# Kernel optimization log

Hardware: AMD Instinct MI355X
Metric: run time of the kernel (lower is better)

## Reference

```python
import jax, jax.numpy as jnp
import numpy as np

DIM = 768
HID = 1536
EPS = 1e-12
SCALE = float(np.sqrt(DIM))


def _layernorm(x, gamma, beta):
    mu = jnp.mean(x, axis=-1, keepdims=True)
    var = jnp.mean(jnp.square(x - mu), axis=-1, keepdims=True)
    return (x - mu) * jax.lax.rsqrt(var + EPS) * gamma + beta


def setup_inputs() -> dict:
    key = jax.random.key(0)
    ks = jax.random.split(key, 16)
    s = 1.0 / np.sqrt(DIM)
    sh = 1.0 / np.sqrt(HID)
    x = jax.random.normal(ks[0], (8, 2048, DIM), dtype=jnp.float32)
    return {
        "x": x,
        "Wq": jax.random.uniform(ks[1], (DIM, DIM), jnp.float32, -s, s),
        "bq": jax.random.uniform(ks[2], (DIM,), jnp.float32, -s, s),
        "Wk": jax.random.uniform(ks[3], (DIM, DIM), jnp.float32, -s, s),
        "bk": jax.random.uniform(ks[4], (DIM,), jnp.float32, -s, s),
        "Wv": jax.random.uniform(ks[5], (DIM, DIM), jnp.float32, -s, s),
        "bv": jax.random.uniform(ks[6], (DIM,), jnp.float32, -s, s),
        "Wp": jax.random.uniform(ks[7], (DIM, DIM), jnp.float32, -s, s),
        "bp": jax.random.uniform(ks[8], (DIM,), jnp.float32, -s, s),
        "g1": jnp.ones((DIM,), jnp.float32),
        "be1": jnp.zeros((DIM,), jnp.float32),
        "W1": jax.random.uniform(ks[9], (HID, DIM), jnp.float32, -s, s),
        "b1": jax.random.uniform(ks[10], (HID,), jnp.float32, -s, s),
        "W2": jax.random.uniform(ks[11], (DIM, HID), jnp.float32, -sh, sh),
        "b2": jax.random.uniform(ks[12], (DIM,), jnp.float32, -sh, sh),
        "g2": jnp.ones((DIM,), jnp.float32),
        "be2": jnp.zeros((DIM,), jnp.float32),
    }


def reference(x, Wq, bq, Wk, bk, Wv, bv, Wp, bp, g1, be1, W1, b1, W2, b2, g2, be2):
    # NOTE: original code does NOT split into heads; single full-dim bmm attention.
    Q = jnp.einsum("bsd,ed->bse", x, Wq) + bq  # [B,S,D]
    K = jnp.einsum("bsd,ed->bse", x, Wk) + bk
    V = jnp.einsum("bsd,ed->bse", x, Wv) + bv
    alpha = jnp.einsum("bqd,bkd->bqk", Q, K) / SCALE  # [B,S,S]
    alpha = jax.nn.softmax(alpha, axis=-1)
    attn = jnp.einsum("bqk,bkd->bqd", alpha, V)
    attn = jnp.einsum("bsd,ed->bse", attn, Wp) + bp  # linear_proj
    h = _layernorm(x + attn, g1, be1)
    mlp = jax.nn.gelu(jnp.einsum("bsd,hd->bsh", h, W1) + b1, approximate=False)
    mlp = jnp.einsum("bsh,dh->bsd", mlp, W2) + b2
    return _layernorm(h + mlp, g2, be2)
```

## Files before the change

### kernel.cpp

```cpp
#include <hip/hip_runtime.h>
#include <math.h>

#define D_MODEL 768
#define D_HID   1536
#define N_BATCH 8
#define SEQLEN  2048
#define NROWS   (N_BATCH*SEQLEN)

typedef unsigned short u16;
typedef __attribute__((ext_vector_type(8))) short bfrag;
typedef __attribute__((ext_vector_type(4))) float facc;

__device__ __forceinline__ u16 f2bf(float f) {
  unsigned u = __float_as_uint(f);
  u += 0x7fffu + ((u >> 16) & 1u);
  return (u16)(u >> 16);
}
__device__ __forceinline__ float bf2f(u16 u) {
  return __uint_as_float((unsigned)u << 16);
}

__device__ __forceinline__ void async16(const void* g, void* l) {
  __builtin_amdgcn_global_load_lds((const __attribute__((address_space(1))) void*)g,
                                   (__attribute__((address_space(3))) void*)l,
                                   16, 0, 0);
}

__global__ __launch_bounds__(256) void cvt_all(
    const float* __restrict__ x,  const float* __restrict__ Wq,
    const float* __restrict__ Wk, const float* __restrict__ Wv,
    const float* __restrict__ Wp, const float* __restrict__ W1,
    const float* __restrict__ W2, const float* __restrict__ bq,
    const float* __restrict__ bk, const float* __restrict__ bv,
    u16* __restrict__ XB, u16* __restrict__ WQKV, u16* __restrict__ WPB,
    u16* __restrict__ W1B, u16* __restrict__ W2B, float* __restrict__ BQKV) {
  long i = (long)blockIdx.x * 256 + threadIdx.x;
  const float* src; u16* dst; long off;
  if      (i < 3145728) { src = x;  dst = XB;             off = i; }
  else if (i < 3293184) { src = Wq; dst = WQKV;           off = i - 3145728; }
  else if (i < 3440640) { src = Wk; dst = WQKV + 589824;  off = i - 3293184; }
  else if (i < 3588096) { src = Wv; dst = WQKV + 1179648; off = i - 3440640; }
  else if (i < 3735552) { src = Wp; dst = WPB;            off = i - 3588096; }
  else if (i < 4030464) { src = W1; dst = W1B;            off = i - 3735552; }
  else if (i < 4325376) { src = W2; dst = W2B;            off = i - 4030464; }
  else if (i < 4325952) {
    long j = i - 4325376;
    const float* s = (j < 192) ? bq : (j < 384) ? bk : bv;
    long o = (j < 192) ? j : (j < 384) ? j - 192 : j - 384;
    ((float4*)BQKV)[j] = ((const float4*)s)[o];
    return;
  } else return;
  float4 v = ((const float4*)src)[off];
  ushort4 o4;
  o4.x = f2bf(v.x); o4.y = f2bf(v.y); o4.z = f2bf(v.z); o4.w = f2bf(v.w);
  *reinterpret_cast<ushort4*>(dst + off * 4) = o4;
}

__global__ __launch_bounds__(256) void transpose_bf16(const u16* __restrict__ in,
                                                      u16* __restrict__ out) {
  __shared__ u16 t[64][68];
  const int z  = blockIdx.z;
  const int bs = blockIdx.x * 64;
  const int bd = blockIdx.y * 64;
  const u16* I = in  + (long)z * SEQLEN * D_MODEL;
  u16*       O = out + (long)z * D_MODEL * SEQLEN;
  const int tt = threadIdx.x;
  const int r = tt >> 2, c4 = (tt & 3) << 4;
#pragma unroll
  for (int k = 0; k < 16; ++k)
    t[r][c4 + k] = I[(long)(bs + r) * D_MODEL + bd + c4 + k];
  __syncthreads();
#pragma unroll
  for (int k = 0; k < 16; ++k)
    O[(long)(bd + r) * SEQLEN + bs + c4 + k] = t[c4 + k][r];
}

enum { EPI_EXP = 1, EPI_DIV = 2, EPI_GELU = 4, EPI_QKV = 5, EPI_RES = 6 };

template<int EPI>
__global__ __launch_bounds__(512, 4)
void gemm_bt(const u16* __restrict__ Aall, const u16* __restrict__ Ball,
             void* __restrict__ Cout,
             int M, int N, int K,
             long sA, long sB, long sC,
             const float* __restrict__ bias,
             const u16* __restrict__ resid,
             float* __restrict__ lsum,
             float scale)
{
  __shared__ __align__(16) char smem[65536];
  u16* As = (u16*)smem;
  u16* Bs = (u16*)(smem + 16384);

  const int z = blockIdx.z;
  const u16* A = Aall + (long)z * sA;
  const u16* B = Ball + (long)z * sB;
  const int bm = blockIdx.x, bn = blockIdx.y;
  const int tid = (int)threadIdx.x;
  const int lane = tid & 63, wv = tid >> 6;
  const int wr = wv >> 2, wc = wv & 3;

  facc acc[4][4] = {};

  const int srow = tid >> 3;
  const int scol = (((tid & 7) ^ (srow & 7)) << 3);
  const u16* Abase = A + (long)(bm * 128) * K;
  const u16* Bbase = B + (long)(bn * 256) * K;

  const int fr = lane & 15;
  const int g0 = lane >> 4;

  for (int k0 = 0; k0 < K; k0 += 64) {
    __syncthreads();
#pragma unroll
    for (int p = 0; p < 2; ++p)
      async16(Abase + (long)(p * 64 + srow) * K + k0 + scol, As + (p * 512 + wv * 64) * 8);
#pragma unroll
    for (int p = 0; p < 4; ++p)
      async16(Bbase + (long)(p * 64 + srow) * K + k0 + scol, Bs + (p * 512 + wv * 64) * 8);
    __syncthreads();
#pragma unroll
    for (int h = 0; h < 2; ++h) {
      bfrag af[4], bfv[4];
      const int gh = g0 + h * 4;
#pragma unroll
      for (int i = 0; i < 4; ++i) {
        const int r = wr * 64 + i * 16 + fr;
        af[i] = *(const bfrag*)(As + r * 64 + ((gh ^ (r & 7)) << 3));
      }
#pragma unroll
      for (int j = 0; j < 4; ++j) {
        const int r = wc * 64 + j * 16 + fr;
        bfv[j] = *(const bfrag*)(Bs + r * 64 + ((gh ^ (r & 7)) << 3));
      }
#pragma unroll
      for (int i = 0; i < 4; ++i)
#pragma unroll
        for (int j = 0; j < 4; ++j)
          acc[i][j] = __builtin_amdgcn_mfma_f32_16x16x32_bf16(af[i], bfv[j], acc[i][j], 0, 0, 0);
    }
  }

  __syncthreads();
  const int rb = bm * 128 + wr * 64;
  const int cb = bn * 256 + wc * 64;
  const int quad = lane >> 4;

  if constexpr (EPI == EPI_RES) {
    float* ep32 = (float*)(smem + wv * 8192);
    u16* Cg = (u16*)Cout;
#pragma unroll
    for (int h = 0; h < 2; ++h) {
#pragma unroll
      for (int i2 = 0; i2 < 2; ++i2) {
        const int i = h * 2 + i2;
#pragma unroll
        for (int r = 0; r < 4; ++r) {
          const int lrow = i2 * 16 + quad * 4 + r;
#pragma unroll
          for (int j = 0; j < 4; ++j)
            ep32[lrow * 64 + j * 16 + fr] = acc[i][j][r];
        }
      }
#pragma unroll
      for (int it = 0; it < 8; ++it) {
        const int lr = it * 4 + (lane >> 4);
        const int ch = (lane & 15) << 2;
        float4 d = *(const float4*)(ep32 + lr * 64 + ch);
        const int row = rb + h * 32 + lr;
        const int gcol = cb + ch;
        const long gi = (long)row * N + gcol;
        ushort4 rv = *(const ushort4*)(resid + gi);
        float4 bb = *(const float4*)(bias + gcol);
        ushort4 o;
        o.x = f2bf(d.x + bb.x + bf2f(rv.x));
        o.y = f2bf(d.y + bb.y + bf2f(rv.y));
        o.z = f2bf(d.z + bb.z + bf2f(rv.z));
        o.w = f2bf(d.w + bb.w + bf2f(rv.w));
        *reinterpret_cast<ushort4*>(Cg + gi) = o;
      }
    }
  } else {
    u16* ep16 = (u16*)(smem + wv * 8192);
    u16* Cg;
    int cbo, rowstride;
    if constexpr (EPI == EPI_QKV) {
      const int c64 = bn * 4 + wc;
      const int which = c64 / 12;
      Cg = (u16*)Cout + (long)which * NROWS * D_MODEL;
      cbo = (c64 - which * 12) * 64;
      rowstride = D_MODEL;
    } else {
      Cg = (u16*)Cout + (long)z * sC;
      cbo = cb;
      rowstride = N;
    }
    float bj[4];
    if constexpr (EPI == EPI_GELU || EPI == EPI_QKV) {
#pragma unroll
      for (int j = 0; j < 4; ++j) bj[j] = bias[cb + j * 16 + fr];
    }
#pragma unroll
    for (int i = 0; i < 4; ++i) {
#pragma unroll
      for (int r = 0; r < 4; ++r) {
        const int lrow = i * 16 + quad * 4 + r;
        const int row = rb + lrow;
        float rs = 0.f;
        float inv = 0.f;
        if constexpr (EPI == EPI_DIV) inv = 1.f / lsum[(long)z * M + row];
#pragma unroll
        for (int j = 0; j < 4; ++j) {
          float v = acc[i][j][r];
          float outv;
          if constexpr (EPI == EPI_EXP) {
            outv = __expf(v * scale);
            rs += outv;
          } else if constexpr (EPI == EPI_DIV) {
            outv = v * inv;
          } else if constexpr (EPI == EPI_QKV) {
            outv = v + bj[j];
          } else {
            float t = v + bj[j];
            outv = 0.5f * t * (1.f + erff(t * 0.70710678f));
          }
          ep16[lrow * 64 + j * 16 + fr] = f2bf(outv);
        }
        if constexpr (EPI == EPI_EXP) {
          rs += __shfl_xor(rs, 1);
          rs += __shfl_xor(rs, 2);
          rs += __shfl_xor(rs, 4);
          rs += __shfl_xor(rs, 8);
          if (fr == 0) atomicAdd(&lsum[(long)z * M + row], rs);
        }
      }
    }
#pragma unroll
    for (int it = 0; it < 8; ++it) {
      const int lr = it * 8 + (lane >> 3);
      const int ch = (lane & 7) << 3;
      int4 d = *(const int4*)(ep16 + lr * 64 + ch);
      *reinterpret_cast<int4*>(Cg + (long)(rb + lr) * rowstride + cbo + ch) = d;
    }
  }
}

__global__ __launch_bounds__(192) void layernorm_rows(const u16* __restrict__ in,
                                                      const float* __restrict__ gamma,
                                                      const float* __restrict__ beta,
                                                      float* __restrict__ outf,
                                                      u16* __restrict__ outb) {
  const int row = blockIdx.x;
  const int t = threadIdx.x;
  ushort4 uv = ((const ushort4*)(in + (long)row * D_MODEL))[t];
  float v0 = bf2f(uv.x), v1 = bf2f(uv.y), v2 = bf2f(uv.z), v3 = bf2f(uv.w);
  float s1 = v0 + v1 + v2 + v3;
  float s2 = v0 * v0 + v1 * v1 + v2 * v2 + v3 * v3;
#pragma unroll
  for (int o = 32; o; o >>= 1) { s1 += __shfl_xor(s1, o); s2 += __shfl_xor(s2, o); }
  __shared__ float r1[3], r2[3];
  const int wv = t >> 6, ln = t & 63;
  if (ln == 0) { r1[wv] = s1; r2[wv] = s2; }
  __syncthreads();
  s1 = r1[0] + r1[1] + r1[2];
  s2 = r2[0] + r2[1] + r2[2];
  const float mu = s1 * (1.f / 768.f);
  const float var = s2 * (1.f / 768.f) - mu * mu;
  const float rstd = rsqrtf(var + 1e-12f);
  float4 gv = ((const float4*)gamma)[t];
  float4 bv = ((const float4*)beta)[t];
  float o0 = (v0 - mu) * rstd * gv.x + bv.x;
  float o1 = (v1 - mu) * rstd * gv.y + bv.y;
  float o2 = (v2 - mu) * rstd * gv.z + bv.z;
  float o3 = (v3 - mu) * rstd * gv.w + bv.w;
  if (outf) {
    float4 ov = {o0, o1, o2, o3};
    ((float4*)(outf + (long)row * D_MODEL))[t] = ov;
  }
  if (outb) {
    ushort4 ob;
    ob.x = f2bf(o0); ob.y = f2bf(o1); ob.z = f2bf(o2); ob.w = f2bf(o3);
    ((ushort4*)(outb + (long)row * D_MODEL))[t] = ob;
  }
}

static const size_t OFF_WP   = 0;
static const size_t OFF_W1   = 1179648;
static const size_t OFF_W2   = 3538944;
static const size_t OFF_LSUM = 5898240;
static const size_t OFF_BQKV = 5963776;
static const size_t OFF_QB   = 6291456;
static const size_t OFF_KB   = 31457280;
static const size_t OFF_VB   = 56623104;
static const size_t OFF_VT   = 81788928;
static const size_t OFF_EB   = 106954752;
static const size_t OFF_XB   = 174063616;
static const size_t OFF_WQKV = 199229440;

extern "C" void kernel_launch(void* const* d_in, const int* in_sizes, int n_in,
                              void* d_out, int out_size, void* d_ws, size_t ws_size,
                              hipStream_t stream) {
  const float* x   = (const float*)d_in[0];
  const float* Wq  = (const float*)d_in[1];
  const float* bq  = (const float*)d_in[2];
  const float* Wk  = (const float*)d_in[3];
  const float* bk  = (const float*)d_in[4];
  const float* Wv  = (const float*)d_in[5];
  const float* bv  = (const float*)d_in[6];
  const float* Wp  = (const float*)d_in[7];
  const float* bp  = (const float*)d_in[8];
  const float* g1  = (const float*)d_in[9];
  const float* be1 = (const float*)d_in[10];
  const float* W1  = (const float*)d_in[11];
  const float* b1  = (const float*)d_in[12];
  const float* W2  = (const float*)d_in[13];
  const float* b2  = (const float*)d_in[14];
  const float* g2  = (const float*)d_in[15];
  const float* be2 = (const float*)d_in[16];

  char* ws = (char*)d_ws;
  u16*   WPB  = (u16*)(ws + OFF_WP);
  u16*   W1B  = (u16*)(ws + OFF_W1);
  u16*   W2B  = (u16*)(ws + OFF_W2);
  float* LSUM = (float*)(ws + OFF_LSUM);
  float* BQKV = (float*)(ws + OFF_BQKV);
  u16*   QB   = (u16*)(ws + OFF_QB);
  u16*   KB   = (u16*)(ws + OFF_KB);
  u16*   VB   = (u16*)(ws + OFF_VB);
  u16*   VT   = (u16*)(ws + OFF_VT);
  u16*   EB   = (u16*)(ws + OFF_EB);
  u16*   XB   = (u16*)(ws + OFF_XB);
  u16*   WQKV = (u16*)(ws + OFF_WQKV);
  u16*   CTX  = (u16*)(ws + OFF_VB);
  u16*   PB   = (u16*)(ws + OFF_QB);
  u16*   HB   = (u16*)(ws + OFF_EB);
  u16*   M1B  = (u16*)(ws + OFF_QB);
  u16*   M2B  = (u16*)(ws + OFF_VT);

  dim3 blk(256), blkg(512), blkl(192);

  cvt_all<<<dim3(16899), blk, 0, stream>>>(x, Wq, Wk, Wv, Wp, W1, W2, bq, bk, bv,
                                           XB, WQKV, WPB, W1B, W2B, BQKV);
  hipMemsetAsync(LSUM, 0, NROWS * sizeof(float), stream);

  gemm_bt<EPI_QKV><<<dim3(128, 9, 1), blkg, 0, stream>>>(XB, WQKV, QB,
      NROWS, 3 * D_MODEL, D_MODEL, 0, 0, 0, BQKV, nullptr, nullptr, 0.f);
  transpose_bf16<<<dim3(SEQLEN / 64, D_MODEL / 64, N_BATCH), blk, 0, stream>>>(VB, VT);

  const float sc = 1.0f / sqrtf((float)D_MODEL);
  gemm_bt<EPI_EXP><<<dim3(16, 8, 8), blkg, 0, stream>>>(QB, KB, EB,
      SEQLEN, SEQLEN, D_MODEL,
      (long)SEQLEN * D_MODEL, (long)SEQLEN * D_MODEL, (long)SEQLEN * SEQLEN,
      nullptr, nullptr, LSUM, sc);
  gemm_bt<EPI_DIV><<<dim3(16, 3, 8), blkg, 0, stream>>>(EB, VT, CTX,
      SEQLEN, D_MODEL, SEQLEN,
      (long)SEQLEN * SEQLEN, (long)D_MODEL * SEQLEN, (long)SEQLEN * D_MODEL,
      nullptr, nullptr, LSUM, 0.f);
  gemm_bt<EPI_RES><<<dim3(128, 3, 1), blkg, 0, stream>>>(CTX, WPB, PB,
      NROWS, D_MODEL, D_MODEL, 0, 0, 0, bp, XB, nullptr, 0.f);
  layernorm_rows<<<dim3(NROWS), blkl, 0, stream>>>(PB, g1, be1, nullptr, HB);
  gemm_bt<EPI_GELU><<<dim3(128, 6, 1), blkg, 0, stream>>>(HB, W1B, M1B,
      NROWS, D_HID, D_MODEL, 0, 0, 0, b1, nullptr, nullptr, 0.f);
  gemm_bt<EPI_RES><<<dim3(128, 3, 1), blkg, 0, stream>>>(M1B, W2B, M2B,
      NROWS, D_MODEL, D_HID, 0, 0, 0, b2, HB, nullptr, 0.f);
  layernorm_rows<<<dim3(NROWS), blkl, 0, stream>>>(M2B, g2, be2, (float*)d_out, nullptr);

  (void)in_sizes; (void)n_in; (void)out_size; (void)ws_size;
}
```

Before: 485.3 us.

## Fuse V transpose into QKV epilogue and use 128x128 tiles for N=768 GEMMs

The QKV GEMM epilogue now writes the V third directly in transposed [dim][seq] layout, which removes the separate transpose kernel and one round trip of V through global memory. A new 256-thread gemm_bt128 kernel with 128x128 tiles and 32KB LDS replaces the 128x256 kernel for the three GEMMs with N=768, doubling their grid size so the CUs are better filled. In exchange, the transposed V stores are narrow strided 8-byte writes, and the smaller tiles reuse each loaded operand less.

```diff
diff --git a/kernel.cpp b/kernel.cpp
--- a/kernel.cpp
+++ b/kernel.cpp
@@ -56,25 +56,6 @@
   *reinterpret_cast<ushort4*>(dst + off * 4) = o4;
 }
 
-__global__ __launch_bounds__(256) void transpose_bf16(const u16* __restrict__ in,
-                                                      u16* __restrict__ out) {
-  __shared__ u16 t[64][68];
-  const int z  = blockIdx.z;
-  const int bs = blockIdx.x * 64;
-  const int bd = blockIdx.y * 64;
-  const u16* I = in  + (long)z * SEQLEN * D_MODEL;
-  u16*       O = out + (long)z * D_MODEL * SEQLEN;
-  const int tt = threadIdx.x;
-  const int r = tt >> 2, c4 = (tt & 3) << 4;
-#pragma unroll
-  for (int k = 0; k < 16; ++k)
-    t[r][c4 + k] = I[(long)(bs + r) * D_MODEL + bd + c4 + k];
-  __syncthreads();
-#pragma unroll
-  for (int k = 0; k < 16; ++k)
-    O[(long)(bd + r) * SEQLEN + bs + c4 + k] = t[c4 + k][r];
-}
-
 enum { EPI_EXP = 1, EPI_DIV = 2, EPI_GELU = 4, EPI_QKV = 5, EPI_RES = 6 };
 
 template<int EPI>
@@ -144,6 +125,165 @@
   __syncthreads();
   const int rb = bm * 128 + wr * 64;
   const int cb = bn * 256 + wc * 64;
+  const int quad = lane >> 4;
+
+  if constexpr (EPI == EPI_QKV) {
+    const int c64 = bn * 4 + wc;
+    const int which = c64 / 12;
+    float bj[4];
+#pragma unroll
+    for (int j = 0; j < 4; ++j) bj[j] = bias[cb + j * 16 + fr];
+    if (which == 2) {
+      u16* VT_ = (u16*)resid;
+      const int zb = rb >> 11;
+      const int seqb = (rb & 2047) + quad * 4;
+      const int dimb = (c64 - 24) * 64;
+#pragma unroll
+      for (int i = 0; i < 4; ++i) {
+#pragma unroll
+        for (int j = 0; j < 4; ++j) {
+          const int dim = dimb + j * 16 + fr;
+          ushort4 o;
+          o.x = f2bf(acc[i][j][0] + bj[j]);
+          o.y = f2bf(acc[i][j][1] + bj[j]);
+          o.z = f2bf(acc[i][j][2] + bj[j]);
+          o.w = f2bf(acc[i][j][3] + bj[j]);
+          *reinterpret_cast<ushort4*>(VT_ + (long)zb * D_MODEL * SEQLEN +
+                                      (long)dim * SEQLEN + seqb + i * 16) = o;
+        }
+      }
+      return;
+    }
+    u16* ep16 = (u16*)(smem + wv * 8192);
+    u16* Cg = (u16*)Cout + (long)which * NROWS * D_MODEL;
+    const int cbo = (c64 - which * 12) * 64;
+#pragma unroll
+    for (int i = 0; i < 4; ++i)
+#pragma unroll
+      for (int r = 0; r < 4; ++r) {
+        const int lrow = i * 16 + quad * 4 + r;
+#pragma unroll
+        for (int j = 0; j < 4; ++j)
+          ep16[lrow * 64 + j * 16 + fr] = f2bf(acc[i][j][r] + bj[j]);
+      }
+#pragma unroll
+    for (int it = 0; it < 8; ++it) {
+      const int lr = it * 8 + (lane >> 3);
+      const int ch = (lane & 7) << 3;
+      int4 d = *(const int4*)(ep16 + lr * 64 + ch);
+      *reinterpret_cast<int4*>(Cg + (long)(rb + lr) * D_MODEL + cbo + ch) = d;
+    }
+  } else {
+    u16* ep16 = (u16*)(smem + wv * 8192);
+    u16* Cg = (u16*)Cout + (long)z * sC;
+    float bj[4];
+    if constexpr (EPI == EPI_GELU) {
+#pragma unroll
+      for (int j = 0; j < 4; ++j) bj[j] = bias[cb + j * 16 + fr];
+    }
+#pragma unroll
+    for (int i = 0; i < 4; ++i) {
+#pragma unroll
+      for (int r = 0; r < 4; ++r) {
+        const int lrow = i * 16 + quad * 4 + r;
+        const int row = rb + lrow;
+        float rs = 0.f;
+#pragma unroll
+        for (int j = 0; j < 4; ++j) {
+          float v = acc[i][j][r];
+          float outv;
+          if constexpr (EPI == EPI_EXP) {
+            outv = __expf(v * scale);
+            rs += outv;
+          } else {
+            float t = v + bj[j];
+            outv = 0.5f * t * (1.f + erff(t * 0.70710678f));
+          }
+          ep16[lrow * 64 + j * 16 + fr] = f2bf(outv);
+        }
+        if constexpr (EPI == EPI_EXP) {
+          rs += __shfl_xor(rs, 1);
+          rs += __shfl_xor(rs, 2);
+          rs += __shfl_xor(rs, 4);
+          rs += __shfl_xor(rs, 8);
+          if (fr == 0) atomicAdd(&lsum[(long)z * M + row], rs);
+        }
+      }
+    }
+#pragma unroll
+    for (int it = 0; it < 8; ++it) {
+      const int lr = it * 8 + (lane >> 3);
+      const int ch = (lane & 7) << 3;
+      int4 d = *(const int4*)(ep16 + lr * 64 + ch);
+      *reinterpret_cast<int4*>(Cg + (long)(rb + lr) * N + cb + ch) = d;
+    }
+  }
+}
+
+template<int EPI>
+__global__ __launch_bounds__(256, 5)
+void gemm_bt128(const u16* __restrict__ Aall, const u16* __restrict__ Ball,
+                void* __restrict__ Cout,
+                int M, int N, int K,
+                long sA, long sB, long sC,
+                const float* __restrict__ bias,
+                const u16* __restrict__ resid,
+                float* __restrict__ lsum,
+                float scale)
+{
+  __shared__ __align__(16) char smem[32768];
+  u16* As = (u16*)smem;
+  u16* Bs = (u16*)(smem + 16384);
+
+  const int z = blockIdx.z;
+  const u16* A = Aall + (long)z * sA;
+  const u16* B = Ball + (long)z * sB;
+  const int bm = blockIdx.x, bn = blockIdx.y;
+  const int tid = (int)threadIdx.x;
+  const int lane = tid & 63, wv = tid >> 6;
+  const int wr = wv >> 1, wc = wv & 1;
+
+  facc acc[4][4] = {};
+
+  const int srow = tid >> 3;
+  const int scol = (((tid & 7) ^ (srow & 7)) << 3);
+  const u16* Abase = A + (long)(bm * 128) * K;
+  const u16* Bbase = B + (long)(bn * 128) * K;
+  const int fr = lane & 15, g0 = lane >> 4;
+
+  for (int k0 = 0; k0 < K; k0 += 64) {
+    __syncthreads();
+#pragma unroll
+    for (int p = 0; p < 4; ++p) {
+      async16(Abase + (long)(p * 32 + srow) * K + k0 + scol, As + (p * 256 + wv * 64) * 8);
+      async16(Bbase + (long)(p * 32 + srow) * K + k0 + scol, Bs + (p * 256 + wv * 64) * 8);
+    }
+    __syncthreads();
+#pragma unroll
+    for (int h = 0; h < 2; ++h) {
+      bfrag af[4], bfv[4];
+      const int gh = g0 + h * 4;
+#pragma unroll
+      for (int i = 0; i < 4; ++i) {
+        const int r = wr * 64 + i * 16 + fr;
+        af[i] = *(const bfrag*)(As + r * 64 + ((gh ^ (r & 7)) << 3));
+      }
+#pragma unroll
+      for (int j = 0; j < 4; ++j) {
+        const int r = wc * 64 + j * 16 + fr;
+        bfv[j] = *(const bfrag*)(Bs + r * 64 + ((gh ^ (r & 7)) << 3));
+      }
+#pragma unroll
+      for (int i = 0; i < 4; ++i)
+#pragma unroll
+        for (int j = 0; j < 4; ++j)
+          acc[i][j] = __builtin_amdgcn_mfma_f32_16x16x32_bf16(af[i], bfv[j], acc[i][j], 0, 0, 0);
+    }
+  }
+
+  __syncthreads();
+  const int rb = bm * 128 + wr * 64;
+  const int cb = bn * 128 + wc * 64;
   const int quad = lane >> 4;
 
   if constexpr (EPI == EPI_RES) {
@@ -182,57 +322,17 @@
     }
   } else {
     u16* ep16 = (u16*)(smem + wv * 8192);
-    u16* Cg;
-    int cbo, rowstride;
-    if constexpr (EPI == EPI_QKV) {
-      const int c64 = bn * 4 + wc;
-      const int which = c64 / 12;
-      Cg = (u16*)Cout + (long)which * NROWS * D_MODEL;
-      cbo = (c64 - which * 12) * 64;
-      rowstride = D_MODEL;
-    } else {
-      Cg = (u16*)Cout + (long)z * sC;
-      cbo = cb;
-      rowstride = N;
-    }
-    float bj[4];
-    if constexpr (EPI == EPI_GELU || EPI == EPI_QKV) {
-#pragma unroll
-      for (int j = 0; j < 4; ++j) bj[j] = bias[cb + j * 16 + fr];
-    }
+    u16* Cg = (u16*)Cout + (long)z * sC;
 #pragma unroll
     for (int i = 0; i < 4; ++i) {
 #pragma unroll
       for (int r = 0; r < 4; ++r) {
         const int lrow = i * 16 + quad * 4 + r;
         const int row = rb + lrow;
-        float rs = 0.f;
-        float inv = 0.f;
-        if constexpr (EPI == EPI_DIV) inv = 1.f / lsum[(long)z * M + row];
-#pragma unroll
-        for (int j = 0; j < 4; ++j) {
-          float v = acc[i][j][r];
-          float outv;
-          if constexpr (EPI == EPI_EXP) {
-            outv = __expf(v * scale);
-            rs += outv;
-          } else if constexpr (EPI == EPI_DIV) {
-            outv = v * inv;
-          } else if constexpr (EPI == EPI_QKV) {
-            outv = v + bj[j];
-          } else {
-            float t = v + bj[j];
-            outv = 0.5f * t * (1.f + erff(t * 0.70710678f));
-          }
-          ep16[lrow * 64 + j * 16 + fr] = f2bf(outv);
-        }
-        if constexpr (EPI == EPI_EXP) {
-          rs += __shfl_xor(rs, 1);
-          rs += __shfl_xor(rs, 2);
-          rs += __shfl_xor(rs, 4);
-          rs += __shfl_xor(rs, 8);
-          if (fr == 0) atomicAdd(&lsum[(long)z * M + row], rs);
-        }
+        const float inv = 1.f / lsum[(long)z * M + row];
+#pragma unroll
+        for (int j = 0; j < 4; ++j)
+          ep16[lrow * 64 + j * 16 + fr] = f2bf(acc[i][j][r] * inv);
       }
     }
 #pragma unroll
@@ -240,7 +340,7 @@
       const int lr = it * 8 + (lane >> 3);
       const int ch = (lane & 7) << 3;
       int4 d = *(const int4*)(ep16 + lr * 64 + ch);
-      *reinterpret_cast<int4*>(Cg + (long)(rb + lr) * rowstride + cbo + ch) = d;
+      *reinterpret_cast<int4*>(Cg + (long)(rb + lr) * N + cb + ch) = d;
     }
   }
 }
@@ -326,7 +426,6 @@
   float* BQKV = (float*)(ws + OFF_BQKV);
   u16*   QB   = (u16*)(ws + OFF_QB);
   u16*   KB   = (u16*)(ws + OFF_KB);
-  u16*   VB   = (u16*)(ws + OFF_VB);
   u16*   VT   = (u16*)(ws + OFF_VT);
   u16*   EB   = (u16*)(ws + OFF_EB);
   u16*   XB   = (u16*)(ws + OFF_XB);
@@ -344,24 +443,23 @@
   hipMemsetAsync(LSUM, 0, NROWS * sizeof(float), stream);
 
   gemm_bt<EPI_QKV><<<dim3(128, 9, 1), blkg, 0, stream>>>(XB, WQKV, QB,
-      NROWS, 3 * D_MODEL, D_MODEL, 0, 0, 0, BQKV, nullptr, nullptr, 0.f);
-  transpose_bf16<<<dim3(SEQLEN / 64, D_MODEL / 64, N_BATCH), blk, 0, stream>>>(VB, VT);
+      NROWS, 3 * D_MODEL, D_MODEL, 0, 0, 0, BQKV, VT, nullptr, 0.f);
 
   const float sc = 1.0f / sqrtf((float)D_MODEL);
   gemm_bt<EPI_EXP><<<dim3(16, 8, 8), blkg, 0, stream>>>(QB, KB, EB,
       SEQLEN, SEQLEN, D_MODEL,
       (long)SEQLEN * D_MODEL, (long)SEQLEN * D_MODEL, (long)SEQLEN * SEQLEN,
       nullptr, nullptr, LSUM, sc);
-  gemm_bt<EPI_DIV><<<dim3(16, 3, 8), blkg, 0, stream>>>(EB, VT, CTX,
+  gemm_bt128<EPI_DIV><<<dim3(16, 6, 8), blk, 0, stream>>>(EB, VT, CTX,
       SEQLEN, D_MODEL, SEQLEN,
       (long)SEQLEN * SEQLEN, (long)D_MODEL * SEQLEN, (long)SEQLEN * D_MODEL,
       nullptr, nullptr, LSUM, 0.f);
-  gemm_bt<EPI_RES><<<dim3(128, 3, 1), blkg, 0, stream>>>(CTX, WPB, PB,
+  gemm_bt128<EPI_RES><<<dim3(128, 6, 1), blk, 0, stream>>>(CTX, WPB, PB,
       NROWS, D_MODEL, D_MODEL, 0, 0, 0, bp, XB, nullptr, 0.f);
   layernorm_rows<<<dim3(NROWS), blkl, 0, stream>>>(PB, g1, be1, nullptr, HB);
   gemm_bt<EPI_GELU><<<dim3(128, 6, 1), blkg, 0, stream>>>(HB, W1B, M1B,
       NROWS, D_HID, D_MODEL, 0, 0, 0, b1, nullptr, nullptr, 0.f);
-  gemm_bt<EPI_RES><<<dim3(128, 3, 1), blkg, 0, stream>>>(M1B, W2B, M2B,
+  gemm_bt128<EPI_RES><<<dim3(128, 6, 1), blk, 0, stream>>>(M1B, W2B, M2B,
       NROWS, D_MODEL, D_HID, 0, 0, 0, b2, HB, nullptr, 0.f);
   layernorm_rows<<<dim3(NROWS), blkl, 0, stream>>>(M2B, g2, be2, (float*)d_out, nullptr);
 
```

New measurement: 666.0 us. 37.2% more time.
